# Performance work log

Measured on AMD Instinct MI355X. Metric: run time of the kernel, lower is better.

## Reference

```python
import jax, jax.numpy as jnp
import numpy as np

H = 8
DH = 64
SCALE = DH ** -0.5

def setup_inputs() -> dict:
    key = jax.random.key(0)
    ks = jax.random.split(key, 32)
    B, NQ, N1, N2, N3 = 4, 1024, 1024, 1024, 2048
    QD, C1, C2, C3 = 512, 512, 768, 256
    INNER, VD = H * DH, 512
    s = 0.02
    inp = {
        'x':        jax.random.normal(ks[0], (B, NQ, QD), jnp.float32),
        'context':  jax.random.normal(ks[1], (B, N1, C1), jnp.float32),
        'context2': jax.random.normal(ks[2], (B, N2, C2), jnp.float32),
        'context3': jax.random.normal(ks[3], (B, N3, C3), jnp.float32),
        'mask1': jax.random.randint(ks[4], (B, NQ, N1), 0, 2) > 0,
        'mask2': jax.random.randint(ks[5], (B, NQ, N2), 0, 2) > 0,
        'mask3': jax.random.randint(ks[6], (B, NQ, N3), 0, 2) > 0,
        'Wq':  jax.random.normal(ks[7],  (QD, INNER), jnp.float32) * s,
        'bq':  jnp.zeros((INNER,), jnp.float32),
        'Wk1': jax.random.normal(ks[8],  (C1, INNER), jnp.float32) * s,
        'bk1': jnp.zeros((INNER,), jnp.float32),
        'Wv1': jax.random.normal(ks[9],  (C1, VD), jnp.float32) * s,
        'bv1': jnp.zeros((VD,), jnp.float32),
        'Wk2': jax.random.normal(ks[10], (C2, INNER), jnp.float32) * s,
        'bk2': jnp.zeros((INNER,), jnp.float32),
        'Wv2': jax.random.normal(ks[11], (C2, VD), jnp.float32) * s,
        'bv2': jnp.zeros((VD,), jnp.float32),
        'Wk3': jax.random.normal(ks[12], (C3, INNER), jnp.float32) * s,
        'bk3': jnp.zeros((INNER,), jnp.float32),
        'Wv3': jax.random.normal(ks[13], (C3, VD), jnp.float32) * s,
        'bv3': jnp.zeros((VD,), jnp.float32),
        'Wo':  jax.random.normal(ks[14], (VD, VD), jnp.float32) * s,
        'bo':  jnp.zeros((VD,), jnp.float32),
    }
    return inp

def _split_heads(t):
    # [b, n, h*d] -> [b, h, n, d]
    b, n, hd = t.shape
    return t.reshape(b, n, H, hd // H).transpose(0, 2, 1, 3)

def reference(x, context, context2, context3, mask1, mask2, mask3,
              Wq, bq, Wk1, bk1, Wv1, bv1, Wk2, bk2, Wv2, bv2,
              Wk3, bk3, Wv3, bv3, Wo, bo):
    q = x @ Wq + bq
    k = jnp.concatenate([context @ Wk1 + bk1, context2 @ Wk2 + bk2, context3 @ Wk3 + bk3], axis=1)
    v = jnp.concatenate([context @ Wv1 + bv1, context2 @ Wv2 + bv2, context3 @ Wv3 + bv3], axis=1)
    qh, kh, vh = _split_heads(q), _split_heads(k), _split_heads(v)
    sim = jnp.einsum('bhid,bhjd->bhij', qh, kh) * SCALE  # [b,h,nq,nk]
    mask = jnp.concatenate([mask1, mask2, mask3], axis=2)  # [b,nq,nk]
    neg = -jnp.finfo(sim.dtype).max
    sim = jnp.where(mask[:, None, :, :], sim, neg)
    attn = jax.nn.softmax(sim, axis=-1)
    out = jnp.einsum('bhij,bhjd->bhid', attn, vh)  # [b,h,nq,dv]
    b, h, n, d = out.shape
    out = out.transpose(0, 2, 1, 3).reshape(b, n, h * d)
    return out @ Wo + bo
```

## Files before the change

kernel.cpp:

```cpp
#include <hip/hip_runtime.h>

typedef _Float16 f16;
typedef _Float16 f16x8 __attribute__((ext_vector_type(8)));
typedef _Float16 f16x4 __attribute__((ext_vector_type(4)));
typedef _Float16 f16x2 __attribute__((ext_vector_type(2)));
typedef float f32x4 __attribute__((ext_vector_type(4)));
typedef unsigned long long u64;

#define MFMA16(a, b, c) __builtin_amdgcn_mfma_f32_16x16x32_f16((a), (b), (c), 0, 0, 0)

constexpr float QSCALE = 0.18033688011112042f;

__device__ __forceinline__ void gll16(const f16* g, f16* l) {
  __builtin_amdgcn_global_load_lds((__attribute__((address_space(1))) void*)(g),
                                   (__attribute__((address_space(3))) void*)(l),
                                   16, 0, 0);
}

struct CDesc { const float* src; f16* dst; unsigned n4, off4; };
struct TDesc { const float* src; f16* dst; int K, blk_off; };

struct PrepArgs {
  const void* m1; const void* m2; const void* m3; u64* mb;
  CDesc cd[4];
  TDesc td[8];
};

__global__ __launch_bounds__(256) void prep_kernel(PrepArgs a) {
  int bid = blockIdx.x;
  int tid = threadIdx.x;
  __shared__ float tile[32][33];
  if (bid < 16384) {
    int l = tid & 63;
    unsigned probe = ((const unsigned*)a.m1)[tid & 15];
    u64 vote = __ballot(probe <= 1u);
    bool int_mode = ((vote & 0xFFFFull) == 0xFFFFull);
    unsigned gw = bid * 4u + (tid >> 6);
    unsigned e0 = gw * 256u;
    unsigned row = e0 >> 12, j0 = e0 & 4095;
    const void* src; size_t base;
    if (j0 < 1024) { src = a.m1; base = (size_t)row * 1024 + j0; }
    else if (j0 < 2048) { src = a.m2; base = (size_t)row * 1024 + (j0 - 1024); }
    else { src = a.m3; base = (size_t)row * 2048 + (j0 - 2048); }
    u64 b0, b1, b2, b3;
    if (int_mode) {
      const int* s = (const int*)src + base + l;
      b0 = __ballot(s[0] != 0);   b1 = __ballot(s[64] != 0);
      b2 = __ballot(s[128] != 0); b3 = __ballot(s[192] != 0);
    } else {
      const unsigned char* s = (const unsigned char*)src + base + l;
      b0 = __ballot(s[0] != 0);   b1 = __ballot(s[64] != 0);
      b2 = __ballot(s[128] != 0); b3 = __ballot(s[192] != 0);
    }
    u64 b = b0;
    if (l == 1) b = b1; else if (l == 2) b = b2; else if (l == 3) b = b3;
    if (l < 4) a.mb[gw * 4 + l] = b;
    return;
  }
  if (bid < 25600) {
    unsigned t = (bid - 16384) * 256u + tid;
    CDesc s;
    if (t >= a.cd[3].off4) s = a.cd[3];
    else if (t >= a.cd[2].off4) s = a.cd[2];
    else if (t >= a.cd[1].off4) s = a.cd[1];
    else s = a.cd[0];
    unsigned i = t - s.off4;
    if (i >= s.n4) return;
    float4 v = ((const float4*)s.src)[i];
    f16x4 o;
    o[0] = (f16)v.x; o[1] = (f16)v.y; o[2] = (f16)v.z; o[3] = (f16)v.w;
    ((f16x4*)s.dst)[i] = o;
    return;
  }
  int tb = bid - 25600;
  int di = 0;
#pragma unroll
  for (int i = 1; i < 8; i++)
    if (tb >= a.td[i].blk_off) di = i;
  TDesc d = a.td[di];
  int lb = tb - d.blk_off;
  int ktiles = d.K >> 5;
  int kt = lb % ktiles, nt = lb / ktiles;
  int k0 = kt * 32, n0 = nt * 32;
  int tc = tid & 31, tr = tid >> 5;
#pragma unroll
  for (int i = 0; i < 4; i++) {
    int kl = tr + 8 * i;
    tile[tc][kl] = d.src[(size_t)(k0 + kl) * 512 + n0 + tc];
  }
  __syncthreads();
#pragma unroll
  for (int i = 0; i < 4; i++) {
    int nl = tr + 8 * i;
    d.dst[(size_t)(n0 + nl) * d.K + k0 + tc] = (f16)tile[nl][tc];
  }
}

struct PDesc {
  const f16* A; const f16* B; const float* bias; void* out;
  int K, mode, logNloc, nk_off, blk_off, ntiles;
};
struct PArgs { PDesc d[8]; };

__global__ __launch_bounds__(256) void proj_kernel(PArgs args, int bid_base) {
  int bid = blockIdx.x + bid_base;
  int di = 0;
#pragma unroll
  for (int i = 1; i < 8; i++)
    if (bid >= args.d[i].blk_off) di = i;
  PDesc d = args.d[di];
  int lb = bid - d.blk_off;
  int bn = lb % d.ntiles, bm = lb / d.ntiles;
  int tid = threadIdx.x;
  int lane = tid & 63, wv = tid >> 6;
  int wm = wv >> 1, wn = wv & 1;
  int r16 = lane & 15, q4 = lane >> 4;
  int K = d.K;
  int m0 = bm * 128, n0 = bn * 128;

  __shared__ f16 As[2][128 * 32];
  __shared__ f16 Bs[2][128 * 32];

  int srow = 32 * wv + (lane >> 2);
  int scol = 8 * (lane & 3);
  const f16* agw = d.A + (size_t)(m0 + srow) * K + scol;
  const f16* bgw = d.B + (size_t)(n0 + srow) * K + scol;
  auto stage = [&](int p, int kk) {
#pragma unroll
    for (int cc = 0; cc < 2; cc++) {
      gll16(agw + (size_t)(16 * cc) * K + kk, As[p] + 1024 * wv + 512 * cc);
      gll16(bgw + (size_t)(16 * cc) * K + kk, Bs[p] + 1024 * wv + 512 * cc);
    }
  };

  f32x4 c[4][4] = {};
  int nk = K >> 5;
  stage(0, 0);
  __syncthreads();
  for (int kt = 0; kt < nk; kt++) {
    int p = kt & 1;
    if (kt + 1 < nk) stage(p ^ 1, (kt + 1) << 5);
    const f16* ab = As[p] + (wm * 64 + r16) * 32 + q4 * 8;
    const f16* bb = Bs[p] + (wn * 64 + r16) * 32 + q4 * 8;
    f16x8 af[4], bf[4];
#pragma unroll
    for (int t = 0; t < 4; t++) af[t] = *(const f16x8*)(ab + t * 16 * 32);
#pragma unroll
    for (int u = 0; u < 4; u++) bf[u] = *(const f16x8*)(bb + u * 16 * 32);
#pragma unroll
    for (int t = 0; t < 4; t++)
#pragma unroll
      for (int u = 0; u < 4; u++) c[t][u] = MFMA16(af[t], bf[u], c[t][u]);
    __syncthreads();
  }

  int msk = (1 << d.logNloc) - 1;
#pragma unroll
  for (int t = 0; t < 4; t++) {
#pragma unroll
    for (int u = 0; u < 4; u++) {
#pragma unroll
      for (int r = 0; r < 4; r++) {
        int gm = m0 + wm * 64 + t * 16 + q4 * 4 + r;
        int cn = n0 + wn * 64 + u * 16 + r16;
        float val = c[t][u][r] + (d.mode == 2 ? d.bias[gm] : d.bias[cn]);
        if (d.mode == 0) {
          int hh = cn >> 6, dd = cn & 63, bb = gm >> 10, nn = gm & 1023;
          ((f16*)d.out)[(((size_t)bb * 8 + hh) * 1024 + nn) * 64 + dd] = (f16)(val * QSCALE);
        } else if (d.mode == 1) {
          int hh = cn >> 6, dd = cn & 63, bb = gm >> d.logNloc, nn = d.nk_off + (gm & msk);
          ((f16*)d.out)[(((size_t)bb * 8 + hh) * 4096 + nn) * 64 + dd] = (f16)val;
        } else if (d.mode == 2) {
          int hh = gm >> 6, dd = gm & 63, bb = cn >> d.logNloc, nn = d.nk_off + (cn & msk);
          ((f16*)d.out)[(((size_t)bb * 8 + hh) * 64 + dd) * 4096 + nn] = (f16)val;
        } else {
          ((float*)d.out)[(size_t)gm * 512 + cn] = val;
        }
      }
    }
  }
}

__global__ __launch_bounds__(256, 3) void attn_kernel(const f16* __restrict__ Qh,
                                                      const f16* __restrict__ Kh,
                                                      const f16* __restrict__ Vt,
                                                      const u64* __restrict__ MB,
                                                      f16* __restrict__ PO,
                                                      float* __restrict__ LW) {
  int lin = blockIdx.x;
  int hb = lin & 31;
  int rest = lin >> 5;
  int qt = rest & 7, ks = rest >> 3;
  int h = hb & 7, b = hb >> 3;
  int tid = threadIdx.x;
  int lane = tid & 63, wv = tid >> 6;
  int r16 = lane & 15, q4 = lane >> 4;
  int q0 = qt * 128;
  int bh = b * 8 + h;

  const f16* qp = Qh + ((size_t)bh * 1024 + q0 + wv * 32) * 64;
  f16x8 aq[2][2];
#pragma unroll
  for (int s = 0; s < 2; s++) {
    aq[s][0] = *(const f16x8*)(qp + (s * 16 + r16) * 64 + q4 * 8);
    aq[s][1] = *(const f16x8*)(qp + (s * 16 + r16) * 64 + q4 * 8 + 32);
  }
  const f16* kg = Kh + (size_t)bh * (4096 * 64) + (size_t)ks * 1024 * 64;
  const f16* vg = Vt + (size_t)bh * (64 * 4096) + ks * 1024;
  const u64* mrow = MB + ((size_t)b * 1024 + q0 + wv * 32 + r16) * 64 + ks * 16;

  __shared__ f16 kls[2][64 * 64];
  __shared__ f16 vls[2][64 * 64];
  __shared__ f16 pbuf[4][32 * 40];
  f16* pw = pbuf[wv];

  int Tv = wv >> 1, hlf = wv & 1;
  int row0 = 32 * hlf + (lane >> 3);
  int blk = (lane & 7) ^ ((lane >> 3) & 7);
  const f16* kgw = kg + (size_t)row0 * 64 + 8 * blk;
  const f16* vgw = vg + (size_t)row0 * 4096 + 8 * blk;
  auto stage = [&](int pp, int j0) {
    if (Tv == 0) {
      const f16* g = kgw + (size_t)j0 * 64;
      f16* l = kls[pp] + 2048 * hlf;
#pragma unroll
      for (int cc = 0; cc < 4; cc++) gll16(g + cc * (8 * 64), l + cc * 512);
    } else {
      const f16* g = vgw + j0;
      f16* l = vls[pp] + 2048 * hlf;
#pragma unroll
      for (int cc = 0; cc < 4; cc++) gll16(g + (size_t)cc * (8 * 4096), l + cc * 512);
    }
  };

  f16x8 ones;
#pragma unroll
  for (int i = 0; i < 8; i++) ones[i] = (f16)1.0f;
  f32x4 accl[2] = {};
  f32x4 acc[2][4] = {};

  stage(0, 0);
  __syncthreads();

  int sw = 8 * (r16 & 7);
  for (int jt = 0; jt < 16; jt++) {
    int p = jt & 1;
    u64 wrd[2];
    wrd[0] = mrow[jt];
    wrd[1] = mrow[16 * 64 + jt];
    if (jt < 15) stage(p ^ 1, (jt + 1) * 64);
    const f16* kb_ = kls[p];
    const f16* vb_ = vls[p];
#pragma unroll
    for (int ph = 0; ph < 2; ph++) {
#pragma unroll
      for (int th = 0; th < 2; th++) {
        int t = ph * 2 + th;
        f16x8 k0 = *(const f16x8*)(kb_ + (t * 16 + r16) * 64 + ((q4 * 8) ^ sw));
        f16x8 k1 = *(const f16x8*)(kb_ + (t * 16 + r16) * 64 + ((32 + q4 * 8) ^ sw));
#pragma unroll
        for (int s = 0; s < 2; s++) {
          f32x4 z{};
          z = MFMA16(k0, aq[s][0], z);
          z = MFMA16(k1, aq[s][1], z);
          u64 w = wrd[s] >> (t * 16 + q4 * 4);
          float p0 = (w & 1) ? __builtin_amdgcn_exp2f(z[0]) : 0.0f;
          float p1 = (w & 2) ? __builtin_amdgcn_exp2f(z[1]) : 0.0f;
          float p2 = (w & 4) ? __builtin_amdgcn_exp2f(z[2]) : 0.0f;
          float p3 = (w & 8) ? __builtin_amdgcn_exp2f(z[3]) : 0.0f;
          f16x2 lo = __builtin_bit_cast(f16x2, __builtin_amdgcn_cvt_pkrtz(p0, p1));
          f16x2 hi = __builtin_bit_cast(f16x2, __builtin_amdgcn_cvt_pkrtz(p2, p3));
          f16x4 pk = __builtin_shufflevector(lo, hi, 0, 1, 2, 3);
          *(f16x4*)(pw + (s * 16 + r16) * 40 + th * 16 + q4 * 4) = pk;
        }
      }
      asm volatile("s_waitcnt lgkmcnt(0)" ::: "memory");
      f16x8 ap[2];
#pragma unroll
      for (int s = 0; s < 2; s++)
        ap[s] = *(const f16x8*)(pw + (s * 16 + r16) * 40 + q4 * 8);
#pragma unroll
      for (int dt = 0; dt < 4; dt++) {
        f16x8 vf = *(const f16x8*)(vb_ + (dt * 16 + r16) * 64 + ((ph * 32 + q4 * 8) ^ sw));
#pragma unroll
        for (int s = 0; s < 2; s++) acc[s][dt] = MFMA16(ap[s], vf, acc[s][dt]);
      }
#pragma unroll
      for (int s = 0; s < 2; s++) accl[s] = MFMA16(ap[s], ones, accl[s]);
    }
    __syncthreads();
  }

  f16* pok = PO + (size_t)ks * (4096 * 512);
#pragma unroll
  for (int s = 0; s < 2; s++)
#pragma unroll
    for (int r = 0; r < 4; r++) {
      int rowg = b * 1024 + q0 + wv * 32 + s * 16 + q4 * 4 + r;
      f16* orow = pok + (size_t)rowg * 512 + h * 64 + r16;
#pragma unroll
      for (int dt = 0; dt < 4; dt++) orow[dt * 16] = (f16)(acc[s][dt][r]);
    }
  if (r16 == 0) {
    float* lk = LW + (size_t)ks * 32768 + (size_t)bh * 1024 + q0 + wv * 32;
#pragma unroll
    for (int s = 0; s < 2; s++)
#pragma unroll
      for (int r = 0; r < 4; r++) lk[s * 16 + q4 * 4 + r] = accl[s][r];
  }
}

__global__ __launch_bounds__(256) void combine_kernel(const f16* __restrict__ PO,
                                                      const float* __restrict__ LW,
                                                      f16* __restrict__ AO) {
  int t = blockIdx.x * 256 + threadIdx.x;
  int row = t >> 6;
  int col = (t & 63) * 8;
  int b = row >> 10, q = row & 1023;
  int h = col >> 6;
  size_t lidx = (size_t)(b * 8 + h) * 1024 + q;
  float l = LW[lidx] + LW[32768 + lidx] + LW[65536 + lidx] + LW[98304 + lidx];
  float inv = 1.0f / l;
  size_t off = (size_t)row * 512 + col;
  f16x8 o0 = *(const f16x8*)(PO + off);
  f16x8 o1 = *(const f16x8*)(PO + 2097152 + off);
  f16x8 o2 = *(const f16x8*)(PO + 4194304 + off);
  f16x8 o3 = *(const f16x8*)(PO + 6291456 + off);
  f16x8 out;
#pragma unroll
  for (int j = 0; j < 8; j++)
    out[j] = (f16)(((float)o0[j] + (float)o1[j] + (float)o2[j] + (float)o3[j]) * inv);
  *(f16x8*)(AO + off) = out;
}

extern "C" void kernel_launch(void* const* d_in, const int* in_sizes, int n_in,
                              void* d_out, int out_size, void* d_ws, size_t ws_size,
                              hipStream_t stream) {
  (void)in_sizes; (void)n_in; (void)out_size; (void)ws_size;
  const float* x  = (const float*)d_in[0];
  const float* c1 = (const float*)d_in[1];
  const float* c2 = (const float*)d_in[2];
  const float* c3 = (const float*)d_in[3];
  const void* m1 = d_in[4];
  const void* m2 = d_in[5];
  const void* m3 = d_in[6];
  const float* Wq = (const float*)d_in[7];   const float* bq = (const float*)d_in[8];
  const float* Wk1 = (const float*)d_in[9];  const float* bk1 = (const float*)d_in[10];
  const float* Wv1 = (const float*)d_in[11]; const float* bv1 = (const float*)d_in[12];
  const float* Wk2 = (const float*)d_in[13]; const float* bk2 = (const float*)d_in[14];
  const float* Wv2 = (const float*)d_in[15]; const float* bv2 = (const float*)d_in[16];
  const float* Wk3 = (const float*)d_in[17]; const float* bk3 = (const float*)d_in[18];
  const float* Wv3 = (const float*)d_in[19]; const float* bv3 = (const float*)d_in[20];
  const float* Wo = (const float*)d_in[21];  const float* bo = (const float*)d_in[22];

  char* ws = (char*)d_ws;
  size_t off = 0;
  auto alloc = [&](size_t bytes) {
    void* p = ws + off;
    off = (off + bytes + 255) & ~(size_t)255;
    return p;
  };
  f16* xb   = (f16*)alloc(2097152 * 2);
  f16* c1b  = (f16*)alloc(2097152 * 2);
  f16* c2b  = (f16*)alloc(3145728 * 2);
  f16* c3b  = (f16*)alloc(2097152 * 2);
  f16* wqt  = (f16*)alloc(262144 * 2);
  f16* wk1t = (f16*)alloc(262144 * 2);
  f16* wk2t = (f16*)alloc(393216 * 2);
  f16* wk3t = (f16*)alloc(131072 * 2);
  f16* wv1t = (f16*)alloc(262144 * 2);
  f16* wv2t = (f16*)alloc(393216 * 2);
  f16* wv3t = (f16*)alloc(131072 * 2);
  f16* wot  = (f16*)alloc(262144 * 2);
  f16* qh   = (f16*)alloc(2097152 * 2);
  f16* kh   = (f16*)alloc(8388608 * 2);
  f16* vt   = (f16*)alloc(8388608 * 2);
  f16* ao   = (f16*)alloc(2097152 * 2);
  u64* mbits = (u64*)alloc(2097152);

  f16* po = (f16*)ws;
  float* lw = (float*)(ws + 16777216);

  PrepArgs pra;
  pra.m1 = m1; pra.m2 = m2; pra.m3 = m3; pra.mb = mbits;
  pra.cd[0] = {x,  xb,  524288, 0};
  pra.cd[1] = {c1, c1b, 524288, 524288};
  pra.cd[2] = {c2, c2b, 786432, 1048576};
  pra.cd[3] = {c3, c3b, 524288, 1835008};
  pra.td[0] = {Wq,  wqt,  512, 0};
  pra.td[1] = {Wk1, wk1t, 512, 256};
  pra.td[2] = {Wk2, wk2t, 768, 512};
  pra.td[3] = {Wk3, wk3t, 256, 896};
  pra.td[4] = {Wv1, wv1t, 512, 1024};
  pra.td[5] = {Wv2, wv2t, 768, 1280};
  pra.td[6] = {Wv3, wv3t, 256, 1664};
  pra.td[7] = {Wo,  wot,  512, 1792};
  prep_kernel<<<27648, 256, 0, stream>>>(pra);

  PArgs pa;
  pa.d[0] = {xb,   wqt,  bq,  qh,    512, 0, 10, 0,    0,    4};
  pa.d[1] = {c1b,  wk1t, bk1, kh,    512, 1, 10, 0,    128,  4};
  pa.d[2] = {c2b,  wk2t, bk2, kh,    768, 1, 10, 1024, 256,  4};
  pa.d[3] = {c3b,  wk3t, bk3, kh,    256, 1, 11, 2048, 384,  4};
  pa.d[4] = {wv1t, c1b,  bv1, vt,    512, 2, 10, 0,    640,  32};
  pa.d[5] = {wv2t, c2b,  bv2, vt,    768, 2, 10, 1024, 768,  32};
  pa.d[6] = {wv3t, c3b,  bv3, vt,    256, 2, 11, 2048, 896,  64};
  pa.d[7] = {ao,   wot,  bo,  d_out, 512, 3, 10, 0,    1152, 4};
  proj_kernel<<<1152, 256, 0, stream>>>(pa, 0);

  attn_kernel<<<1024, 256, 0, stream>>>(qh, kh, vt, mbits, po, lw);

  combine_kernel<<<1024, 256, 0, stream>>>(po, lw, ao);

  proj_kernel<<<128, 256, 0, stream>>>(pa, 1152);
}
```

Measured before the change: 324.8 us.

## Fuse split-K combine into output projection and use padded register-staged K/V tiles

Removes the separate combine kernel by folding the four partial attention outputs and their normalisation into the A-tile staging of the output projection GEMM. That stage now loads from global into registers and writes to LDS instead of using direct global-to-LDS loads. Separately, the attention kernel replaces the XOR-swizzled direct-to-LDS K/V staging with register prefetch two tiles ahead into a padded (stride 72) LDS layout. This saves one launch and an intermediate buffer round trip. In exchange, the output GEMM does redundant combine work for each N tile, and the attention kernel uses more registers and a synchronous LDS write path.

Result: slower. 334.8 us (+3.1%).

```diff
diff --git a/kernel.cpp b/kernel.cpp
--- a/kernel.cpp
+++ b/kernel.cpp
@@ -102,7 +102,9 @@
 };
 struct PArgs { PDesc d[8]; };
 
-__global__ __launch_bounds__(256) void proj_kernel(PArgs args, int bid_base) {
+__global__ __launch_bounds__(256) void proj_kernel(PArgs args, int bid_base,
+                                                   const f16* __restrict__ PO,
+                                                   const float* __restrict__ LW) {
   int bid = blockIdx.x + bid_base;
   int di = 0;
 #pragma unroll
@@ -125,10 +127,31 @@
   int scol = 8 * (lane & 3);
   const f16* agw = d.A + (size_t)(m0 + srow) * K + scol;
   const f16* bgw = d.B + (size_t)(n0 + srow) * K + scol;
+  bool fuse = (d.mode == 3);
   auto stage = [&](int p, int kk) {
 #pragma unroll
     for (int cc = 0; cc < 2; cc++) {
-      gll16(agw + (size_t)(16 * cc) * K + kk, As[p] + 1024 * wv + 512 * cc);
+      if (!fuse) {
+        gll16(agw + (size_t)(16 * cc) * K + kk, As[p] + 1024 * wv + 512 * cc);
+      } else {
+        int r = m0 + srow + 16 * cc;
+        int col = kk + scol;
+        int bb = r >> 10, q = r & 1023;
+        int h = col >> 6;
+        size_t lidx = (size_t)(bb * 8 + h) * 1024 + q;
+        float l = LW[lidx] + LW[32768 + lidx] + LW[65536 + lidx] + LW[98304 + lidx];
+        float inv = 1.0f / l;
+        size_t poff = (size_t)r * 512 + col;
+        f16x8 o0 = *(const f16x8*)(PO + poff);
+        f16x8 o1 = *(const f16x8*)(PO + 2097152 + poff);
+        f16x8 o2 = *(const f16x8*)(PO + 4194304 + poff);
+        f16x8 o3 = *(const f16x8*)(PO + 6291456 + poff);
+        f16x8 cmb;
+#pragma unroll
+        for (int j = 0; j < 8; j++)
+          cmb[j] = (f16)(((float)o0[j] + (float)o1[j] + (float)o2[j] + (float)o3[j]) * inv);
+        *(f16x8*)(As[p] + 1024 * wv + 512 * cc + (lane >> 2) * 32 + scol) = cmb;
+      }
       gll16(bgw + (size_t)(16 * cc) * K + kk, Bs[p] + 1024 * wv + 512 * cc);
     }
   };
@@ -209,28 +232,27 @@
   const f16* vg = Vt + (size_t)bh * (64 * 4096) + ks * 1024;
   const u64* mrow = MB + ((size_t)b * 1024 + q0 + wv * 32 + r16) * 64 + ks * 16;
 
-  __shared__ f16 kls[2][64 * 64];
-  __shared__ f16 vls[2][64 * 64];
+  __shared__ f16 kls[2][64 * 72];
+  __shared__ f16 vls[2][64 * 72];
   __shared__ f16 pbuf[4][32 * 40];
   f16* pw = pbuf[wv];
 
-  int Tv = wv >> 1, hlf = wv & 1;
-  int row0 = 32 * hlf + (lane >> 3);
-  int blk = (lane & 7) ^ ((lane >> 3) & 7);
-  const f16* kgw = kg + (size_t)row0 * 64 + 8 * blk;
-  const f16* vgw = vg + (size_t)row0 * 4096 + 8 * blk;
-  auto stage = [&](int pp, int j0) {
-    if (Tv == 0) {
-      const f16* g = kgw + (size_t)j0 * 64;
-      f16* l = kls[pp] + 2048 * hlf;
-#pragma unroll
-      for (int cc = 0; cc < 4; cc++) gll16(g + cc * (8 * 64), l + cc * 512);
-    } else {
-      const f16* g = vgw + j0;
-      f16* l = vls[pp] + 2048 * hlf;
-#pragma unroll
-      for (int cc = 0; cc < 4; cc++) gll16(g + (size_t)cc * (8 * 4096), l + cc * 512);
-    }
+  int c_row = tid >> 3;
+  int c_col = (tid & 7) * 8;
+  f16x8 kr0, kr1, vr0, vr1;
+  auto loadKV = [&](int j0) {
+    const f16* kp = kg + (size_t)(j0 + c_row) * 64 + c_col;
+    kr0 = *(const f16x8*)kp;
+    kr1 = *(const f16x8*)(kp + 32 * 64);
+    const f16* vp = vg + (size_t)c_row * 4096 + j0 + c_col;
+    vr0 = *(const f16x8*)vp;
+    vr1 = *(const f16x8*)(vp + 32 * 4096);
+  };
+  auto writeKV = [&](int p) {
+    *(f16x8*)(kls[p] + c_row * 72 + c_col) = kr0;
+    *(f16x8*)(kls[p] + (c_row + 32) * 72 + c_col) = kr1;
+    *(f16x8*)(vls[p] + c_row * 72 + c_col) = vr0;
+    *(f16x8*)(vls[p] + (c_row + 32) * 72 + c_col) = vr1;
   };
 
   f16x8 ones;
@@ -239,16 +261,18 @@
   f32x4 accl[2] = {};
   f32x4 acc[2][4] = {};
 
-  stage(0, 0);
+  loadKV(0);
+  writeKV(0);
+  loadKV(64);
   __syncthreads();
 
-  int sw = 8 * (r16 & 7);
   for (int jt = 0; jt < 16; jt++) {
     int p = jt & 1;
+    if (jt < 15) writeKV(p ^ 1);
+    if (jt < 14) loadKV((jt + 2) * 64);
     u64 wrd[2];
-    wrd[0] = mrow[jt];
-    wrd[1] = mrow[16 * 64 + jt];
-    if (jt < 15) stage(p ^ 1, (jt + 1) * 64);
+#pragma unroll
+    for (int s = 0; s < 2; s++) wrd[s] = mrow[s * 16 * 64 + jt];
     const f16* kb_ = kls[p];
     const f16* vb_ = vls[p];
 #pragma unroll
@@ -256,8 +280,8 @@
 #pragma unroll
       for (int th = 0; th < 2; th++) {
         int t = ph * 2 + th;
-        f16x8 k0 = *(const f16x8*)(kb_ + (t * 16 + r16) * 64 + ((q4 * 8) ^ sw));
-        f16x8 k1 = *(const f16x8*)(kb_ + (t * 16 + r16) * 64 + ((32 + q4 * 8) ^ sw));
+        f16x8 k0 = *(const f16x8*)(kb_ + (t * 16 + r16) * 72 + q4 * 8);
+        f16x8 k1 = *(const f16x8*)(kb_ + (t * 16 + r16) * 72 + q4 * 8 + 32);
 #pragma unroll
         for (int s = 0; s < 2; s++) {
           f32x4 z{};
@@ -281,7 +305,7 @@
         ap[s] = *(const f16x8*)(pw + (s * 16 + r16) * 40 + q4 * 8);
 #pragma unroll
       for (int dt = 0; dt < 4; dt++) {
-        f16x8 vf = *(const f16x8*)(vb_ + (dt * 16 + r16) * 64 + ((ph * 32 + q4 * 8) ^ sw));
+        f16x8 vf = *(const f16x8*)(vb_ + (dt * 16 + r16) * 72 + ph * 32 + q4 * 8);
 #pragma unroll
         for (int s = 0; s < 2; s++) acc[s][dt] = MFMA16(ap[s], vf, acc[s][dt]);
       }
@@ -308,29 +332,6 @@
 #pragma unroll
       for (int r = 0; r < 4; r++) lk[s * 16 + q4 * 4 + r] = accl[s][r];
   }
-}
-
-__global__ __launch_bounds__(256) void combine_kernel(const f16* __restrict__ PO,
-                                                      const float* __restrict__ LW,
-                                                      f16* __restrict__ AO) {
-  int t = blockIdx.x * 256 + threadIdx.x;
-  int row = t >> 6;
-  int col = (t & 63) * 8;
-  int b = row >> 10, q = row & 1023;
-  int h = col >> 6;
-  size_t lidx = (size_t)(b * 8 + h) * 1024 + q;
-  float l = LW[lidx] + LW[32768 + lidx] + LW[65536 + lidx] + LW[98304 + lidx];
-  float inv = 1.0f / l;
-  size_t off = (size_t)row * 512 + col;
-  f16x8 o0 = *(const f16x8*)(PO + off);
-  f16x8 o1 = *(const f16x8*)(PO + 2097152 + off);
-  f16x8 o2 = *(const f16x8*)(PO + 4194304 + off);
-  f16x8 o3 = *(const f16x8*)(PO + 6291456 + off);
-  f16x8 out;
-#pragma unroll
-  for (int j = 0; j < 8; j++)
-    out[j] = (f16)(((float)o0[j] + (float)o1[j] + (float)o2[j] + (float)o3[j]) * inv);
-  *(f16x8*)(AO + off) = out;
 }
 
 extern "C" void kernel_launch(void* const* d_in, const int* in_sizes, int n_in,
@@ -405,12 +406,10 @@
   pa.d[4] = {wv1t, c1b,  bv1, vt,    512, 2, 10, 0,    640,  32};
   pa.d[5] = {wv2t, c2b,  bv2, vt,    768, 2, 10, 1024, 768,  32};
   pa.d[6] = {wv3t, c3b,  bv3, vt,    256, 2, 11, 2048, 896,  64};
-  pa.d[7] = {ao,   wot,  bo,  d_out, 512, 3, 10, 0,    1152, 4};
-  proj_kernel<<<1152, 256, 0, stream>>>(pa, 0);
+  pa.d[7] = {po,   wot,  bo,  d_out, 512, 3, 10, 0,    1152, 4};
+  proj_kernel<<<1152, 256, 0, stream>>>(pa, 0, po, lw);
 
   attn_kernel<<<1024, 256, 0, stream>>>(qh, kh, vt, mbits, po, lw);
 
-  combine_kernel<<<1024, 256, 0, stream>>>(po, lw, ao);
-
-  proj_kernel<<<128, 256, 0, stream>>>(pa, 1152);
+  proj_kernel<<<128, 256, 0, stream>>>(pa, 1152, po, lw);
 }
```
